# Performance work log

Hardware: AMD Instinct MI355X
Metric: run time of the kernel (lower is better)

## Reference

```python
import jax, jax.numpy as jnp
import numpy as np
from jax import lax

B, T, BYTE_LEN, EMB = 8, 4096, 8, 64
FILTERS = [(1, 4), (2, 8), (3, 12), (4, 16), (5, 20), (6, 24), (7, 28)]
LAST_DIM = sum(c for _, c in FILTERS)  # 112
OUT_DIM = 512


def setup_inputs() -> dict:
    key = jax.random.key(0)
    ks = jax.random.split(key, 32)
    inp = {"features": jax.random.normal(ks[0], (B, T, BYTE_LEN, EMB), dtype=jnp.float32)}
    for i, (w, c) in enumerate(FILTERS):
        inp[f"conv_w{i+1}"] = jax.random.normal(ks[1 + i], (c, EMB, w), dtype=jnp.float32) * 0.05
        inp[f"conv_b{i+1}"] = jax.random.normal(ks[8 + i], (c,), dtype=jnp.float32) * 0.05
    inp["hw_w1"] = jax.random.normal(ks[15], (2 * LAST_DIM, LAST_DIM), dtype=jnp.float32) * 0.05
    inp["hw_b1"] = jnp.concatenate([jnp.zeros(LAST_DIM), jnp.ones(LAST_DIM)]).astype(jnp.float32)
    inp["hw_w2"] = jax.random.normal(ks[16], (2 * LAST_DIM, LAST_DIM), dtype=jnp.float32) * 0.05
    inp["hw_b2"] = jnp.concatenate([jnp.zeros(LAST_DIM), jnp.ones(LAST_DIM)]).astype(jnp.float32)
    inp["proj_w"] = jax.random.normal(ks[17], (OUT_DIM, LAST_DIM), dtype=jnp.float32) * 0.05
    inp["proj_b"] = jax.random.normal(ks[18], (OUT_DIM,), dtype=jnp.float32) * 0.05
    return inp


def _conv_branch(x, w, b):
    # x: [N, EMB, BYTE_LEN], w: [out_c, EMB, width] -> max over time, relu -> [N, out_c]
    y = lax.conv_general_dilated(x, w, window_strides=(1,), padding='VALID',
                                 dimension_numbers=('NCH', 'OIH', 'NCH'))
    y = y + b[None, :, None]
    return jax.nn.relu(jnp.max(y, axis=-1))


def _highway_layer(x, w, b):
    p = x @ w.T + b
    proj_x, gate = jnp.split(p, 2, axis=-1)
    g = jax.nn.sigmoid(gate)
    return g * x + (1.0 - g) * jax.nn.relu(proj_x)


def reference(features, conv_w1, conv_w2, conv_w3, conv_w4, conv_w5, conv_w6, conv_w7,
              conv_b1, conv_b2, conv_b3, conv_b4, conv_b5, conv_b6, conv_b7,
              hw_w1, hw_b1, hw_w2, hw_b2, proj_w, proj_b):
    b, t, byte_len, emb = features.shape
    # transpose(2,3).view(-1, emb, byte_len)
    x = features.transpose(0, 1, 3, 2).reshape(-1, emb, byte_len)  # [B*T, EMB, BYTE_LEN]
    ws = [conv_w1, conv_w2, conv_w3, conv_w4, conv_w5, conv_w6, conv_w7]
    bs = [conv_b1, conv_b2, conv_b3, conv_b4, conv_b5, conv_b6, conv_b7]
    branches = [_conv_branch(x, w, bb) for w, bb in zip(ws, bs)]
    h = jnp.concatenate(branches, axis=-1)  # [B*T, LAST_DIM]
    h = _highway_layer(h, hw_w1, hw_b1)
    h = _highway_layer(h, hw_w2, hw_b2)
    out = h @ proj_w.T + proj_b  # [B*T, OUT_DIM]
    return out.reshape(b, t, -1)
```

## Files before the change

kernel.cpp:

```cpp
#include <hip/hip_runtime.h>

typedef __attribute__((ext_vector_type(8))) short short8;
typedef __attribute__((ext_vector_type(4))) float f32x4;

#define NPOS 32768
#define KDIM 512
#define NCT  30
#define CHUNK_BYTES 30720

__device__ __forceinline__ unsigned short f2bf(float x) {
    unsigned u = __float_as_uint(x);
    return (unsigned short)((u + 0x7FFFu + ((u >> 16) & 1u)) >> 16);
}
__device__ __forceinline__ float bf2f(unsigned short h) {
    return __uint_as_float(((unsigned)h) << 16);
}

__device__ __forceinline__ void stage16(const void* g, void* l, int lane) {
    __builtin_amdgcn_global_load_lds(
        (const __attribute__((address_space(1))) unsigned int*)g,
        (__attribute__((address_space(3))) unsigned int*)l, 16, 0, 0);
}

__global__ void prep_kernel(const float* __restrict__ w1, const float* __restrict__ w2,
                            const float* __restrict__ w3, const float* __restrict__ w4,
                            const float* __restrict__ w5, const float* __restrict__ w6,
                            const float* __restrict__ w7, const float* __restrict__ hw1,
                            const float* __restrict__ hw2, const float* __restrict__ pw,
                            unsigned short* __restrict__ WC, unsigned short* __restrict__ W1s,
                            unsigned short* __restrict__ W2s, unsigned short* __restrict__ Ps) {
    int gid = blockIdx.x * 256 + threadIdx.x;
    if (gid < 245760) {
        int k = gid / 480, col = gid % 480;
        const float* wp; int cbnd, NP, C, W;
        if (col < 32)       { wp = w1; cbnd = 0;   NP = 8; C = 4;  W = 1; }
        else if (col < 96)  { wp = w2; cbnd = 32;  NP = 7; C = 8;  W = 2; }
        else if (col < 176) { wp = w3; cbnd = 96;  NP = 6; C = 12; W = 3; }
        else if (col < 256) { wp = w4; cbnd = 176; NP = 5; C = 16; W = 4; }
        else if (col < 336) { wp = w5; cbnd = 256; NP = 4; C = 20; W = 5; }
        else if (col < 416) { wp = w6; cbnd = 336; NP = 3; C = 24; W = 6; }
        else                { wp = w7; cbnd = 416; NP = 2; C = 28; W = 7; }
        int c2 = col - cbnd, oc = c2 / NP, p = c2 - oc * NP;
        int j = k >> 6, e = k & 63, dk = j - p;
        float v = 0.f;
        if (oc < C && dk >= 0 && dk < W) v = wp[(oc * 64 + e) * W + dk];
        int q = k >> 5, kr = k & 31;
        WC[((q * NCT + (col >> 4)) * 64 + ((kr >> 3) * 16 + (col & 15))) * 8 + (kr & 7)] = f2bf(v);
    } else if (gid < 245760 + 57344) {
        int x = gid - 245760;
        const float* src = (x < 28672) ? hw1 : hw2;
        unsigned short* dst = (x < 28672) ? W1s : W2s;
        if (x >= 28672) x -= 28672;
        int k = x / 224, n = x % 224;
        float v = (k < 112) ? src[n * 112 + k] : 0.f;
        int q = k >> 5, kr = k & 31;
        dst[((q * 14 + (n >> 4)) * 64 + ((kr >> 3) * 16 + (n & 15))) * 8 + (kr & 7)] = f2bf(v);
    } else if (gid < 245760 + 57344 + 65536) {
        int x = gid - 303104;
        int k = x / 512, n = x % 512;
        float v = (k < 112) ? pw[n * 112 + k] : 0.f;
        int q = k >> 5, kr = k & 31;
        Ps[((q * 32 + (n >> 4)) * 64 + ((kr >> 3) * 16 + (n & 15))) * 8 + (kr & 7)] = f2bf(v);
    }
}

template <int T0, int NT>
__device__ __forceinline__ void dump_phase(float* Cb, const f32x4* acc, int wave, int lane) {
    int r0 = wave * 16 + ((lane >> 4) * 4);
    int c0 = lane & 15;
#pragma unroll
    for (int tt = 0; tt < NT; ++tt)
#pragma unroll
        for (int r = 0; r < 4; ++r)
            Cb[(r0 + r) * 161 + tt * 16 + c0] = acc[T0 + tt][r];
}

__device__ void reduce_phase(const float* Cb, unsigned short* ht, int tid,
                             int cA, int NPA, int choffA, int colbA, const float* cbA,
                             int cB, int NPB, int choffB, int colbB, const float* cbB) {
    int noc = cA + cB;
    for (int idx = tid; idx < 64 * noc; idx += 256) {
        int row = idx & 63, ocp = idx >> 6;
        bool isB = ocp >= cA;
        int oc = isB ? ocp - cA : ocp;
        int NP = isB ? NPB : NPA;
        int colb = isB ? colbB : colbA;
        int choff = isB ? choffB : choffA;
        const float* cb = isB ? cbB : cbA;
        const float* src = Cb + row * 161 + colb + oc * NP;
        float m = src[0];
        for (int k = 1; k < NP; ++k) m = fmaxf(m, src[k]);
        float v = fmaxf(m + cb[oc], 0.f);
        ht[row * 136 + choff + oc] = f2bf(v);
    }
}

__global__ __launch_bounds__(256, 2) void fused_kernel(
        const float* __restrict__ feat, const unsigned short* __restrict__ WC,
        const float* cb0, const float* cb1, const float* cb2, const float* cb3,
        const float* cb4, const float* cb5, const float* cb6,
        const unsigned short* __restrict__ W1, const unsigned short* __restrict__ W2,
        const unsigned short* __restrict__ PW,
        const float* __restrict__ hb1, const float* __restrict__ hb2,
        const float* __restrict__ pb, float* __restrict__ out) {
    __shared__ __align__(16) char sm[65536];
    const int tid = threadIdx.x, lane = tid & 63, wave = tid >> 6;
    const int c0 = lane & 15, kq = lane >> 4;
    const int m0 = blockIdx.x * 64;
    f32x4 zero = {0.f, 0.f, 0.f, 0.f};

    const float* arow = feat + (size_t)(m0 + wave * 16 + c0) * KDIM + kq * 8;
    short8 af[16];
#pragma unroll
    for (int q = 0; q < 16; ++q) {
        float t[8];
        *(float4*)(t)     = *(const float4*)(arow + q * 32);
        *(float4*)(t + 4) = *(const float4*)(arow + q * 32 + 4);
        short8 v;
#pragma unroll
        for (int i = 0; i < 8; ++i) v[i] = (short)f2bf(t[i]);
        af[q] = v;
    }

    f32x4 acc[NCT];
#pragma unroll
    for (int t = 0; t < NCT; ++t) acc[t] = zero;

    for (int i = tid; i < 1920; i += 256)
        stage16(WC + i * 8, sm + (i - lane) * 16, lane);

#pragma unroll
    for (int q = 0; q < 16; ++q) {
        __syncthreads();
        if (q < 15) {
            const unsigned short* src = WC + (q + 1) * (CHUNK_BYTES / 2);
            char* dst = sm + ((q + 1) & 1) * CHUNK_BYTES;
            for (int i = tid; i < 1920; i += 256)
                stage16(src + i * 8, dst + (i - lane) * 16, lane);
        }
        const char* bb = sm + (q & 1) * CHUNK_BYTES;
#pragma unroll
        for (int t = 0; t < NCT; ++t) {
            short8 b = *(const short8*)(bb + (t * 64 + lane) * 16);
            acc[t] = __builtin_amdgcn_mfma_f32_16x16x32_bf16(af[q], b, acc[t], 0, 0, 0);
        }
    }

    float* Cb = (float*)sm;
    unsigned short* ht = (unsigned short*)(sm + 41216);
    __syncthreads();
    for (int i = tid; i < 1024; i += 256)
        ht[(i >> 4) * 136 + 112 + (i & 15)] = 0;
    dump_phase<0, 6>(Cb, acc, wave, lane);
    __syncthreads();
    reduce_phase(Cb, ht, tid, 4, 8, 0, 0, cb0, 8, 7, 4, 32, cb1);
    __syncthreads();
    dump_phase<6, 10>(Cb, acc, wave, lane);
    __syncthreads();
    reduce_phase(Cb, ht, tid, 12, 6, 12, 0, cb2, 16, 5, 24, 80, cb3);
    __syncthreads();
    dump_phase<16, 10>(Cb, acc, wave, lane);
    __syncthreads();
    reduce_phase(Cb, ht, tid, 20, 4, 40, 0, cb4, 24, 3, 60, 80, cb5);
    __syncthreads();
    dump_phase<26, 4>(Cb, acc, wave, lane);
    __syncthreads();
    reduce_phase(Cb, ht, tid, 28, 2, 84, 0, cb6, 0, 1, 0, 0, cb6);
    __syncthreads();

    char* wb = sm;
    short8 a2[4];
#pragma unroll
    for (int q = 0; q < 4; ++q)
        a2[q] = *(const short8*)((const char*)ht + (wave * 16 + c0) * 272 + q * 64 + kq * 16);
    for (int i = tid; i < 896; i += 256)
        stage16(W1 + i * 8, wb + (i - lane) * 16, lane);

    f32x4 acc2[14];
#pragma unroll
    for (int t = 0; t < 14; ++t) acc2[t] = zero;
#pragma unroll
    for (int q = 0; q < 4; ++q) {
        __syncthreads();
        if (q < 3) {
            const unsigned short* src = W1 + (q + 1) * 7168;
            char* dst = wb + ((q + 1) & 1) * 14336;
            for (int i = tid; i < 896; i += 256)
                stage16(src + i * 8, dst + (i - lane) * 16, lane);
        }
        const char* bb = wb + (q & 1) * 14336;
#pragma unroll
        for (int t = 0; t < 14; ++t) {
            short8 b = *(const short8*)(bb + (t * 64 + lane) * 16);
            acc2[t] = __builtin_amdgcn_mfma_f32_16x16x32_bf16(a2[q], b, acc2[t], 0, 0, 0);
        }
    }

    for (int i = tid; i < 896; i += 256)
        stage16(W2 + i * 8, wb + (i - lane) * 16, lane);

#pragma unroll
    for (int t = 0; t < 7; ++t) {
        float bp = hb1[t * 16 + c0], bg = hb1[112 + t * 16 + c0];
#pragma unroll
        for (int r = 0; r < 4; ++r) {
            int row = wave * 16 + kq * 4 + r;
            int col = t * 16 + c0;
            float px = acc2[t][r] + bp;
            float gt = acc2[t + 7][r] + bg;
            float g = 1.f / (1.f + __expf(-gt));
            float hres = bf2f(ht[row * 136 + col]);
            ht[row * 136 + col] = f2bf(g * hres + (1.f - g) * fmaxf(px, 0.f));
        }
    }
    __syncthreads();

    short8 a3[4];
#pragma unroll
    for (int q = 0; q < 4; ++q)
        a3[q] = *(const short8*)((const char*)ht + (wave * 16 + c0) * 272 + q * 64 + kq * 16);

    f32x4 acc3[14];
#pragma unroll
    for (int t = 0; t < 14; ++t) acc3[t] = zero;
#pragma unroll
    for (int q = 0; q < 4; ++q) {
        __syncthreads();
        if (q < 3) {
            const unsigned short* src = W2 + (q + 1) * 7168;
            char* dst = wb + ((q + 1) & 1) * 14336;
            for (int i = tid; i < 896; i += 256)
                stage16(src + i * 8, dst + (i - lane) * 16, lane);
        }
        const char* bb = wb + (q & 1) * 14336;
#pragma unroll
        for (int t = 0; t < 14; ++t) {
            short8 b = *(const short8*)(bb + (t * 64 + lane) * 16);
            acc3[t] = __builtin_amdgcn_mfma_f32_16x16x32_bf16(a3[q], b, acc3[t], 0, 0, 0);
        }
    }

#pragma unroll
    for (int t = 0; t < 7; ++t) {
        float bp = hb2[t * 16 + c0], bg = hb2[112 + t * 16 + c0];
#pragma unroll
        for (int r = 0; r < 4; ++r) {
            int row = wave * 16 + kq * 4 + r;
            int col = t * 16 + c0;
            float px = acc3[t][r] + bp;
            float gt = acc3[t + 7][r] + bg;
            float g = 1.f / (1.f + __expf(-gt));
            float hres = bf2f(ht[row * 136 + col]);
            ht[row * 136 + col] = f2bf(g * hres + (1.f - g) * fmaxf(px, 0.f));
        }
    }
    __syncthreads();

    short8 a4[4];
#pragma unroll
    for (int q = 0; q < 4; ++q)
        a4[q] = *(const short8*)((const char*)ht + (wave * 16 + c0) * 272 + q * 64 + kq * 16);

    char* pwb = sm;
    for (int i = tid; i < 1024; i += 256)
        stage16(PW + i * 8, pwb + (i - lane) * 16, lane);

    f32x4 acc4[32];
#pragma unroll
    for (int t = 0; t < 32; ++t) acc4[t] = zero;
#pragma unroll
    for (int c = 0; c < 8; ++c) {
        __syncthreads();
        if (c < 7) {
            const unsigned short* src = PW + (c + 1) * 8192;
            char* dst = pwb + ((c + 1) & 1) * 16384;
            for (int i = tid; i < 1024; i += 256)
                stage16(src + i * 8, dst + (i - lane) * 16, lane);
        }
        const char* bb = pwb + (c & 1) * 16384;
#pragma unroll
        for (int tt = 0; tt < 16; ++tt) {
            short8 b = *(const short8*)(bb + (tt * 64 + lane) * 16);
            acc4[(c & 1) * 16 + tt] =
                __builtin_amdgcn_mfma_f32_16x16x32_bf16(a4[c >> 1], b, acc4[(c & 1) * 16 + tt], 0, 0, 0);
        }
    }

    float* ot = (float*)sm;
#pragma unroll
    for (int half = 0; half < 2; ++half) {
        __syncthreads();
#pragma unroll
        for (int t16 = 0; t16 < 16; ++t16) {
            int col = (half * 16 + t16) * 16 + c0;
            float b = pb[col];
#pragma unroll
            for (int r = 0; r < 4; ++r)
                ot[(wave * 16 + kq * 4 + r) * 256 + t16 * 16 + c0] = acc4[half * 16 + t16][r] + b;
        }
        __syncthreads();
        for (int i = tid; i < 4096; i += 256) {
            int row = i >> 6, c = i & 63;
            *(float4*)(out + (size_t)(m0 + row) * 512 + half * 256 + c * 4) = ((const float4*)ot)[i];
        }
    }
}

extern "C" void kernel_launch(void* const* d_in, const int* in_sizes, int n_in,
                              void* d_out, int out_size, void* d_ws, size_t ws_size,
                              hipStream_t stream) {
    const float* feat = (const float*)d_in[0];
    const float* cw[7];
    const float* cb[7];
    for (int f = 0; f < 7; ++f) {
        cw[f] = (const float*)d_in[1 + 2 * f];
        cb[f] = (const float*)d_in[2 + 2 * f];
    }
    const float* hw_w1 = (const float*)d_in[15];
    const float* hw_b1 = (const float*)d_in[16];
    const float* hw_w2 = (const float*)d_in[17];
    const float* hw_b2 = (const float*)d_in[18];
    const float* pw    = (const float*)d_in[19];
    const float* pb    = (const float*)d_in[20];
    float* out = (float*)d_out;

    char* ws = (char*)d_ws;
    unsigned short* WC  = (unsigned short*)ws;
    unsigned short* W1s = (unsigned short*)(ws + 491520);
    unsigned short* W2s = (unsigned short*)(ws + 548864);
    unsigned short* Ps  = (unsigned short*)(ws + 606208);

    prep_kernel<<<1440, 256, 0, stream>>>(cw[0], cw[1], cw[2], cw[3], cw[4], cw[5], cw[6],
                                          hw_w1, hw_w2, pw, WC, W1s, W2s, Ps);
    fused_kernel<<<512, 256, 0, stream>>>(feat, WC, cb[0], cb[1], cb[2], cb[3], cb[4], cb[5], cb[6],
                                          W1s, W2s, Ps, hw_b1, hw_b2, pb, out);
}
```

Before: 192.8 us.

## Replace block-wide syncs with vmcnt-gated barriers and prefetch next GEMM weights early

Pads every weight chunk to a power-of-two size so each thread issues a fixed number of global-to-LDS loads. Each __syncthreads in the K loops becomes an explicit s_waitcnt vmcnt(N) plus s_barrier, so the prefetch of the next chunk stays in flight while the current chunk is consumed. The first chunk of the second highway weights and of the projection weights is now staged during the previous GEMM's last iteration, and the MFMA loops raise wave priority with s_setprio. The cost is reliance on hand-counted vmcnt values and removed barriers: if the compiler emits a different number of vector-memory ops, the waits become wrong, and the padding makes each chunk load larger.

```diff
diff --git a/kernel.cpp b/kernel.cpp
--- a/kernel.cpp
+++ b/kernel.cpp
@@ -3,10 +3,9 @@
 typedef __attribute__((ext_vector_type(8))) short short8;
 typedef __attribute__((ext_vector_type(4))) float f32x4;
 
-#define NPOS 32768
 #define KDIM 512
 #define NCT  30
-#define CHUNK_BYTES 30720
+#define BCHUNK 32768
 
 __device__ __forceinline__ unsigned short f2bf(float x) {
     unsigned u = __float_as_uint(x);
@@ -45,7 +44,7 @@
         float v = 0.f;
         if (oc < C && dk >= 0 && dk < W) v = wp[(oc * 64 + e) * W + dk];
         int q = k >> 5, kr = k & 31;
-        WC[((q * NCT + (col >> 4)) * 64 + ((kr >> 3) * 16 + (col & 15))) * 8 + (kr & 7)] = f2bf(v);
+        WC[q * 16384 + ((col >> 4) * 64 + ((kr >> 3) * 16 + (col & 15))) * 8 + (kr & 7)] = f2bf(v);
     } else if (gid < 245760 + 57344) {
         int x = gid - 245760;
         const float* src = (x < 28672) ? hw1 : hw2;
@@ -54,7 +53,7 @@
         int k = x / 224, n = x % 224;
         float v = (k < 112) ? src[n * 112 + k] : 0.f;
         int q = k >> 5, kr = k & 31;
-        dst[((q * 14 + (n >> 4)) * 64 + ((kr >> 3) * 16 + (n & 15))) * 8 + (kr & 7)] = f2bf(v);
+        dst[q * 8192 + ((n >> 4) * 64 + ((kr >> 3) * 16 + (n & 15))) * 8 + (kr & 7)] = f2bf(v);
     } else if (gid < 245760 + 57344 + 65536) {
         int x = gid - 303104;
         int k = x / 512, n = x % 512;
@@ -126,24 +125,31 @@
 #pragma unroll
     for (int t = 0; t < NCT; ++t) acc[t] = zero;
 
-    for (int i = tid; i < 1920; i += 256)
+    for (int i = tid; i < 2048; i += 256)
         stage16(WC + i * 8, sm + (i - lane) * 16, lane);
 
 #pragma unroll
     for (int q = 0; q < 16; ++q) {
-        __syncthreads();
         if (q < 15) {
-            const unsigned short* src = WC + (q + 1) * (CHUNK_BYTES / 2);
-            char* dst = sm + ((q + 1) & 1) * CHUNK_BYTES;
-            for (int i = tid; i < 1920; i += 256)
+            const unsigned short* src = WC + (q + 1) * 16384;
+            char* dst = sm + ((q + 1) & 1) * BCHUNK;
+            for (int i = tid; i < 2048; i += 256)
                 stage16(src + i * 8, dst + (i - lane) * 16, lane);
-        }
-        const char* bb = sm + (q & 1) * CHUNK_BYTES;
+            asm volatile("s_waitcnt vmcnt(8)" ::: "memory");
+        } else {
+            asm volatile("s_waitcnt vmcnt(0)" ::: "memory");
+        }
+        __builtin_amdgcn_s_barrier();
+        const char* bb = sm + (q & 1) * BCHUNK;
+        __builtin_amdgcn_s_setprio(1);
 #pragma unroll
         for (int t = 0; t < NCT; ++t) {
             short8 b = *(const short8*)(bb + (t * 64 + lane) * 16);
             acc[t] = __builtin_amdgcn_mfma_f32_16x16x32_bf16(af[q], b, acc[t], 0, 0, 0);
         }
+        __builtin_amdgcn_s_setprio(0);
+        asm volatile("s_waitcnt lgkmcnt(0)" ::: "memory");
+        __builtin_amdgcn_s_barrier();
     }
 
     float* Cb = (float*)sm;
@@ -173,7 +179,7 @@
 #pragma unroll
     for (int q = 0; q < 4; ++q)
         a2[q] = *(const short8*)((const char*)ht + (wave * 16 + c0) * 272 + q * 64 + kq * 16);
-    for (int i = tid; i < 896; i += 256)
+    for (int i = tid; i < 1024; i += 256)
         stage16(W1 + i * 8, wb + (i - lane) * 16, lane);
 
     f32x4 acc2[14];
@@ -181,23 +187,26 @@
     for (int t = 0; t < 14; ++t) acc2[t] = zero;
 #pragma unroll
     for (int q = 0; q < 4; ++q) {
-        __syncthreads();
         if (q < 3) {
-            const unsigned short* src = W1 + (q + 1) * 7168;
-            char* dst = wb + ((q + 1) & 1) * 14336;
-            for (int i = tid; i < 896; i += 256)
+            const unsigned short* src = W1 + (q + 1) * 8192;
+            char* dst = wb + ((q + 1) & 1) * 16384;
+            for (int i = tid; i < 1024; i += 256)
                 stage16(src + i * 8, dst + (i - lane) * 16, lane);
-        }
-        const char* bb = wb + (q & 1) * 14336;
+        } else {
+            for (int i = tid; i < 1024; i += 256)
+                stage16(W2 + i * 8, wb + (i - lane) * 16, lane);
+        }
+        asm volatile("s_waitcnt vmcnt(4)" ::: "memory");
+        __builtin_amdgcn_s_barrier();
+        const char* bb = wb + (q & 1) * 16384;
 #pragma unroll
         for (int t = 0; t < 14; ++t) {
             short8 b = *(const short8*)(bb + (t * 64 + lane) * 16);
             acc2[t] = __builtin_amdgcn_mfma_f32_16x16x32_bf16(a2[q], b, acc2[t], 0, 0, 0);
         }
-    }
-
-    for (int i = tid; i < 896; i += 256)
-        stage16(W2 + i * 8, wb + (i - lane) * 16, lane);
+        asm volatile("s_waitcnt lgkmcnt(0)" ::: "memory");
+        __builtin_amdgcn_s_barrier();
+    }
 
 #pragma unroll
     for (int t = 0; t < 7; ++t) {
@@ -213,7 +222,6 @@
             ht[row * 136 + col] = f2bf(g * hres + (1.f - g) * fmaxf(px, 0.f));
         }
     }
-    __syncthreads();
 
     short8 a3[4];
 #pragma unroll
@@ -225,19 +233,25 @@
     for (int t = 0; t < 14; ++t) acc3[t] = zero;
 #pragma unroll
     for (int q = 0; q < 4; ++q) {
-        __syncthreads();
         if (q < 3) {
-            const unsigned short* src = W2 + (q + 1) * 7168;
-            char* dst = wb + ((q + 1) & 1) * 14336;
-            for (int i = tid; i < 896; i += 256)
+            const unsigned short* src = W2 + (q + 1) * 8192;
+            char* dst = wb + ((q + 1) & 1) * 16384;
+            for (int i = tid; i < 1024; i += 256)
                 stage16(src + i * 8, dst + (i - lane) * 16, lane);
-        }
-        const char* bb = wb + (q & 1) * 14336;
+        } else {
+            for (int i = tid; i < 1024; i += 256)
+                stage16(PW + i * 8, wb + (i - lane) * 16, lane);
+        }
+        asm volatile("s_waitcnt vmcnt(4)" ::: "memory");
+        __builtin_amdgcn_s_barrier();
+        const char* bb = wb + (q & 1) * 16384;
 #pragma unroll
         for (int t = 0; t < 14; ++t) {
             short8 b = *(const short8*)(bb + (t * 64 + lane) * 16);
             acc3[t] = __builtin_amdgcn_mfma_f32_16x16x32_bf16(a3[q], b, acc3[t], 0, 0, 0);
         }
+        asm volatile("s_waitcnt lgkmcnt(0)" ::: "memory");
+        __builtin_amdgcn_s_barrier();
     }
 
 #pragma unroll
@@ -254,7 +268,6 @@
             ht[row * 136 + col] = f2bf(g * hres + (1.f - g) * fmaxf(px, 0.f));
         }
     }
-    __syncthreads();
 
     short8 a4[4];
 #pragma unroll
@@ -262,28 +275,32 @@
         a4[q] = *(const short8*)((const char*)ht + (wave * 16 + c0) * 272 + q * 64 + kq * 16);
 
     char* pwb = sm;
-    for (int i = tid; i < 1024; i += 256)
-        stage16(PW + i * 8, pwb + (i - lane) * 16, lane);
-
     f32x4 acc4[32];
 #pragma unroll
     for (int t = 0; t < 32; ++t) acc4[t] = zero;
 #pragma unroll
     for (int c = 0; c < 8; ++c) {
-        __syncthreads();
         if (c < 7) {
             const unsigned short* src = PW + (c + 1) * 8192;
             char* dst = pwb + ((c + 1) & 1) * 16384;
             for (int i = tid; i < 1024; i += 256)
                 stage16(src + i * 8, dst + (i - lane) * 16, lane);
-        }
+            asm volatile("s_waitcnt vmcnt(4)" ::: "memory");
+        } else {
+            asm volatile("s_waitcnt vmcnt(0)" ::: "memory");
+        }
+        __builtin_amdgcn_s_barrier();
         const char* bb = pwb + (c & 1) * 16384;
+        __builtin_amdgcn_s_setprio(1);
 #pragma unroll
         for (int tt = 0; tt < 16; ++tt) {
             short8 b = *(const short8*)(bb + (tt * 64 + lane) * 16);
             acc4[(c & 1) * 16 + tt] =
                 __builtin_amdgcn_mfma_f32_16x16x32_bf16(a4[c >> 1], b, acc4[(c & 1) * 16 + tt], 0, 0, 0);
         }
+        __builtin_amdgcn_s_setprio(0);
+        asm volatile("s_waitcnt lgkmcnt(0)" ::: "memory");
+        __builtin_amdgcn_s_barrier();
     }
 
     float* ot = (float*)sm;
@@ -326,9 +343,9 @@
 
     char* ws = (char*)d_ws;
     unsigned short* WC  = (unsigned short*)ws;
-    unsigned short* W1s = (unsigned short*)(ws + 491520);
-    unsigned short* W2s = (unsigned short*)(ws + 548864);
-    unsigned short* Ps  = (unsigned short*)(ws + 606208);
+    unsigned short* W1s = (unsigned short*)(ws + 524288);
+    unsigned short* W2s = (unsigned short*)(ws + 589824);
+    unsigned short* Ps  = (unsigned short*)(ws + 655360);
 
     prep_kernel<<<1440, 256, 0, stream>>>(cw[0], cw[1], cw[2], cw[3], cw[4], cw[5], cw[6],
                                           hw_w1, hw_w2, pw, WC, W1s, W2s, Ps);
```

Result: no change. 192.1 us (-0.4%).
